# Optimization experiments

Measured on AMD Instinct MI355X. Metric: run time of the kernel, lower is better.

Reference implementation:

```python
import jax, jax.numpy as jnp
import numpy as np

N_SIDE = 14          # ViT-S/16 on 224x224 -> 14x14 patches
D_BACKBONE = 384
D_MODEL = 512
B_CLIPS = 32
T_FRAMES = 64
BT = B_CLIPS * T_FRAMES
LN_EPS = 1e-5


def setup_inputs() -> dict:
    key = jax.random.key(0)
    k0, k1, k2, k3, k4 = jax.random.split(key, 5)
    patch_tokens = jax.random.normal(k0, (BT, N_SIDE * N_SIDE, D_BACKBONE), dtype=jnp.float32)
    raw = jax.random.uniform(k1, (BT, 4), dtype=jnp.float32)
    # make well-formed boxes: x1<=x2, y1<=y2 (module clamps anyway)
    xy1 = jnp.minimum(raw[:, :2], raw[:, 2:])
    xy2 = jnp.maximum(raw[:, :2], raw[:, 2:])
    bboxes = jnp.concatenate([xy1, xy2], axis=1)
    obj_visible = jax.random.bernoulli(k2, 0.9, (BT,)).astype(jnp.float32)
    W = jax.random.normal(k3, (D_BACKBONE, D_MODEL), dtype=jnp.float32) * 0.02
    b = jnp.zeros((D_MODEL,), dtype=jnp.float32)
    gamma = jnp.ones((D_MODEL,), dtype=jnp.float32)
    beta = jnp.zeros((D_MODEL,), dtype=jnp.float32)
    mask_token = jax.random.normal(k4, (1, D_MODEL), dtype=jnp.float32) * 0.02
    return {"patch_tokens": patch_tokens, "bboxes": bboxes, "obj_visible": obj_visible,
            "B": B_CLIPS, "T": T_FRAMES, "W": W, "b": b, "gamma": gamma, "beta": beta,
            "mask_token": mask_token}


def _roi_mean_pool(patch_tokens, bboxes):
    bt, N, D = patch_tokens.shape
    n = N_SIDE
    grid = patch_tokens.reshape(bt, n, n, D)
    # exact replica of torch index math (clamp -> trunc/ceil -> clamp -> max)
    x1 = jnp.clip(bboxes[:, 0] * n, 0, n - 1).astype(jnp.int32)
    y1 = jnp.clip(bboxes[:, 1] * n, 0, n - 1).astype(jnp.int32)
    x2 = jnp.clip(jnp.ceil(jnp.clip(bboxes[:, 2] * n, 0, n)), 1, n).astype(jnp.int32)
    y2 = jnp.clip(jnp.ceil(jnp.clip(bboxes[:, 3] * n, 0, n)), 1, n).astype(jnp.int32)
    x2 = jnp.maximum(x2, x1 + 1)
    y2 = jnp.maximum(y2, y1 + 1)
    idx = jnp.arange(n)
    my = (idx[None, :] >= y1[:, None]) & (idx[None, :] < y2[:, None])  # [BT, n]
    mx = (idx[None, :] >= x1[:, None]) & (idx[None, :] < x2[:, None])  # [BT, n]
    mask = (my[:, :, None] & mx[:, None, :]).astype(grid.dtype)        # [BT, n, n]
    count = ((y2 - y1) * (x2 - x1)).astype(grid.dtype)                 # >= 1 always
    pooled = jnp.einsum('bhw,bhwd->bd', mask, grid) / count[:, None]
    return pooled


def reference(patch_tokens, bboxes, obj_visible, B, T, W, b, gamma, beta, mask_token):
    pooled = _roi_mean_pool(patch_tokens, bboxes)          # [BT, D_backbone]
    out = pooled @ W + b                                   # [BT, d_model]
    mu = jnp.mean(out, axis=-1, keepdims=True)
    var = jnp.mean(jnp.square(out - mu), axis=-1, keepdims=True)
    out = (out - mu) * jax.lax.rsqrt(var + LN_EPS) * gamma + beta
    vis = obj_visible[:, None]
    out = vis * out + (1.0 - vis) * mask_token             # learnable mask token blend
    return out.reshape(B, T, -1)
```

## Files before the change

### kernel.cpp

```cpp
#include <hip/hip_runtime.h>
#include <hip/hip_bf16.h>

#define N_SIDE 14
#define N_PATCH (N_SIDE * N_SIDE)
#define D_BB 384
#define DQ_BB (D_BB / 4)
#define D_MODEL 512
#define BT_TOTAL 2048
#define LN_EPS 1e-5f
#define PGROUPS 8
#define KSTEPS (D_BB / 32)

typedef __attribute__((ext_vector_type(8))) short bf16x8;
typedef __attribute__((ext_vector_type(4))) float f32x4;

__device__ __forceinline__ unsigned short f2b(float f) {
    unsigned u = __float_as_uint(f);
    return (unsigned short)((u + 0x7FFFu + ((u >> 16) & 1u)) >> 16);
}

__device__ __forceinline__ void add4(float4& a, const float4& b) {
    a.x += b.x; a.y += b.y; a.z += b.z; a.w += b.w;
}

__device__ __forceinline__ void box_params(const float* __restrict__ bboxes, int bt,
                                           int& x1, int& y1, int& wd, int& total) {
    const float bx1 = bboxes[bt * 4 + 0];
    const float by1 = bboxes[bt * 4 + 1];
    const float bx2 = bboxes[bt * 4 + 2];
    const float by2 = bboxes[bt * 4 + 3];
    x1 = (int)fminf(fmaxf(bx1 * (float)N_SIDE, 0.f), (float)(N_SIDE - 1));
    y1 = (int)fminf(fmaxf(by1 * (float)N_SIDE, 0.f), (float)(N_SIDE - 1));
    int x2 = (int)fminf(fmaxf(ceilf(fminf(fmaxf(bx2 * (float)N_SIDE, 0.f), (float)N_SIDE)), 1.f), (float)N_SIDE);
    int y2 = (int)fminf(fmaxf(ceilf(fminf(fmaxf(by2 * (float)N_SIDE, 0.f), (float)N_SIDE)), 1.f), (float)N_SIDE);
    x2 = max(x2, x1 + 1);
    y2 = max(y2, y1 + 1);
    wd = x2 - x1;
    total = wd * (y2 - y1);
}

__global__ __launch_bounds__(768) void pool_kernel(
    const float* __restrict__ patch,
    const float* __restrict__ bboxes,
    const float* __restrict__ W,
    unsigned short* __restrict__ pooled_bf,
    unsigned short* __restrict__ wpack)
{
    const int bt = blockIdx.x;
    const int t  = threadIdx.x;
    const int qd = t % DQ_BB;
    const int g  = t / DQ_BB;

    __shared__ int    off_tab[N_PATCH];
    __shared__ float4 part[PGROUPS][DQ_BB];

    if (bt < 64) {
        const int nt   = bt >> 1;
        const int kh   = bt & 1;
        const int lane = t & 63;
        const int grp  = t >> 6;
        const int ksl  = grp >> 1;
        const int jh   = grp & 1;
        const int ks   = kh * 6 + ksl;
        const int n    = nt * 16 + (lane & 15);
        const int kb   = ks * 32 + (lane >> 4) * 8 + jh * 4;
        ushort4 w4;
        w4.x = f2b(W[(size_t)(kb + 0) * D_MODEL + n]);
        w4.y = f2b(W[(size_t)(kb + 1) * D_MODEL + n]);
        w4.z = f2b(W[(size_t)(kb + 2) * D_MODEL + n]);
        w4.w = f2b(W[(size_t)(kb + 3) * D_MODEL + n]);
        *(ushort4*)(wpack + ((size_t)(nt * KSTEPS + ks) * 64 + lane) * 8 + jh * 4) = w4;
    }

    int x1, y1, wd, total;
    box_params(bboxes, bt, x1, y1, wd, total);
    const float inv_count = 1.f / (float)total;
    const float inv_wd = 1.f / (float)wd;
    const int cell0 = y1 * N_SIDE + x1;

    if (t < total) {
        const int y = (int)(((float)t + 0.5f) * inv_wd);
        const int x = t - y * wd;
        off_tab[t] = (cell0 + y * N_SIDE + x) * (DQ_BB * 16);
    }
    __syncthreads();

    const char* __restrict__ basep =
        (const char*)patch + (size_t)bt * N_PATCH * D_BB * 4 + (size_t)qd * 16;

    float4 acc = make_float4(0.f, 0.f, 0.f, 0.f);
    int c = g;
    for (; c + 3 * PGROUPS < total; c += 4 * PGROUPS) {
        const int o0 = off_tab[c];
        const int o1 = off_tab[c + PGROUPS];
        const int o2 = off_tab[c + 2 * PGROUPS];
        const int o3 = off_tab[c + 3 * PGROUPS];
        const float4 v0 = *(const float4*)(basep + o0);
        const float4 v1 = *(const float4*)(basep + o1);
        const float4 v2 = *(const float4*)(basep + o2);
        const float4 v3 = *(const float4*)(basep + o3);
        acc.x += (v0.x + v1.x) + (v2.x + v3.x);
        acc.y += (v0.y + v1.y) + (v2.y + v3.y);
        acc.z += (v0.z + v1.z) + (v2.z + v3.z);
        acc.w += (v0.w + v1.w) + (v2.w + v3.w);
    }
    for (; c < total; c += PGROUPS) {
        const float4 v = *(const float4*)(basep + off_tab[c]);
        acc.x += v.x; acc.y += v.y; acc.z += v.z; acc.w += v.w;
    }

    part[g][qd] = acc;
    __syncthreads();

    if (t < DQ_BB) {
        float4 s = part[0][t];
#pragma unroll
        for (int p = 1; p < PGROUPS; ++p) add4(s, part[p][t]);
        ushort4 o;
        o.x = f2b(s.x * inv_count);
        o.y = f2b(s.y * inv_count);
        o.z = f2b(s.z * inv_count);
        o.w = f2b(s.w * inv_count);
        *(ushort4*)(pooled_bf + (size_t)bt * D_BB + t * 4) = o;
    }
}

__global__ __launch_bounds__(512) void mfma_ln_kernel(
    const unsigned short* __restrict__ pooled_bf,
    const unsigned short* __restrict__ wpack,
    const float* __restrict__ bias,
    const float* __restrict__ gamma,
    const float* __restrict__ beta,
    const float* __restrict__ mask_tok,
    const float* __restrict__ vis,
    float* __restrict__ out)
{
    const int tid    = threadIdx.x;
    const int ch     = tid >> 6;
    const int lane   = tid & 63;
    const int lane_m = lane & 15;
    const int lane_g = lane >> 4;
    const int mrow0  = blockIdx.x * 16;

    bf16x8 afrag[KSTEPS];
    {
        const unsigned short* Arow = pooled_bf + (size_t)(mrow0 + lane_m) * D_BB + lane_g * 8;
#pragma unroll
        for (int ks = 0; ks < KSTEPS; ++ks)
            afrag[ks] = *(const bf16x8*)(Arow + ks * 32);
    }

    f32x4 acc[4];
#pragma unroll
    for (int nt = 0; nt < 4; ++nt) acc[nt] = (f32x4){0.f, 0.f, 0.f, 0.f};

#pragma unroll
    for (int nt = 0; nt < 4; ++nt) {
        const unsigned short* bp = wpack + ((size_t)((ch * 4 + nt) * KSTEPS) * 64 + lane) * 8;
#pragma unroll
        for (int ks = 0; ks < KSTEPS; ++ks) {
            const bf16x8 b = *(const bf16x8*)(bp + (size_t)ks * 64 * 8);
            acc[nt] = __builtin_amdgcn_mfma_f32_16x16x32_bf16(afrag[ks], b, acc[nt], 0, 0, 0);
        }
    }

    float s[4] = {0.f, 0.f, 0.f, 0.f}, s2[4] = {0.f, 0.f, 0.f, 0.f};
#pragma unroll
    for (int nt = 0; nt < 4; ++nt) {
        const float bs = bias[ch * 64 + nt * 16 + lane_m];
#pragma unroll
        for (int r = 0; r < 4; ++r) {
            const float v = acc[nt][r] + bs;
            acc[nt][r] = v;
            s[r] += v; s2[r] += v * v;
        }
    }
#pragma unroll
    for (int off = 1; off < 16; off <<= 1) {
#pragma unroll
        for (int r = 0; r < 4; ++r) {
            s[r]  += __shfl_xor(s[r],  off);
            s2[r] += __shfl_xor(s2[r], off);
        }
    }

    __shared__ float lns[8][16][2];
    if (lane_m == 0) {
#pragma unroll
        for (int r = 0; r < 4; ++r) {
            lns[ch][lane_g * 4 + r][0] = s[r];
            lns[ch][lane_g * 4 + r][1] = s2[r];
        }
    }
    __syncthreads();

    float mean4[4], rstd4[4], v4[4], iv4[4];
#pragma unroll
    for (int r = 0; r < 4; ++r) {
        const int m = lane_g * 4 + r;
        float S = 0.f, S2 = 0.f;
#pragma unroll
        for (int c = 0; c < 8; ++c) { S += lns[c][m][0]; S2 += lns[c][m][1]; }
        const float mean = S * (1.f / (float)D_MODEL);
        const float var  = S2 * (1.f / (float)D_MODEL) - mean * mean;
        mean4[r] = mean;
        rstd4[r] = rsqrtf(var + LN_EPS);
        const float v = vis[mrow0 + m];
        v4[r] = v; iv4[r] = 1.f - v;
    }

#pragma unroll
    for (int nt = 0; nt < 4; ++nt) {
        const int n = ch * 64 + nt * 16 + lane_m;
        const float gm  = gamma[n];
        const float bt_ = beta[n];
        const float mt  = mask_tok[n];
#pragma unroll
        for (int r = 0; r < 4; ++r) {
            const int row = mrow0 + lane_g * 4 + r;
            const float o = v4[r] * ((acc[nt][r] - mean4[r]) * rstd4[r] * gm + bt_) + iv4[r] * mt;
            out[(size_t)row * D_MODEL + n] = o;
        }
    }
}

extern "C" void kernel_launch(void* const* d_in, const int* in_sizes, int n_in,
                              void* d_out, int out_size, void* d_ws, size_t ws_size,
                              hipStream_t stream) {
    const float* patch  = (const float*)d_in[0];
    const float* bboxes = (const float*)d_in[1];
    const float* vis    = (const float*)d_in[2];
    const float* W      = (const float*)d_in[5];
    const float* bias   = (const float*)d_in[6];
    const float* gamma  = (const float*)d_in[7];
    const float* beta   = (const float*)d_in[8];
    const float* mtok   = (const float*)d_in[9];

    unsigned short* pooled_bf = (unsigned short*)d_ws;
    unsigned short* wpack     = (unsigned short*)((char*)d_ws + (2u << 20));
    float* out = (float*)d_out;

    pool_kernel<<<BT_TOTAL, 768, 0, stream>>>(patch, bboxes, W, pooled_bf, wpack);
    mfma_ln_kernel<<<BT_TOTAL / 16, 512, 0, stream>>>(
        pooled_bf, wpack, bias, gamma, beta, mtok, vis, out);
}
```

Before: 32.12 us.

## Fuse ROI pooling into MFMA+LayerNorm kernel with 4 rows per block

Moves the W bf16 packing into a small separate kernel. ROI mean pooling now runs inside the GEMM/LayerNorm kernel: each block pools 4 rows sequentially into shared memory, zero-pads them to a 16-row MFMA tile, and writes only the 4 valid rows. This removes the pooled intermediate round-trip through global memory. In exchange, the gather runs with fewer threads per row, behind serial barriers, and 12 of the 16 MFMA rows do wasted work.

```diff
diff --git a/kernel.cpp b/kernel.cpp
--- a/kernel.cpp
+++ b/kernel.cpp
@@ -8,8 +8,9 @@
 #define D_MODEL 512
 #define BT_TOTAL 2048
 #define LN_EPS 1e-5f
-#define PGROUPS 8
 #define KSTEPS (D_BB / 32)
+#define PGR 5
+#define ALDS_P 392
 
 typedef __attribute__((ext_vector_type(8))) short bf16x8;
 typedef __attribute__((ext_vector_type(4))) float f32x4;
@@ -39,31 +40,24 @@
     total = wd * (y2 - y1);
 }
 
-__global__ __launch_bounds__(768) void pool_kernel(
-    const float* __restrict__ patch,
-    const float* __restrict__ bboxes,
+__global__ __launch_bounds__(192) void wpack_kernel(
     const float* __restrict__ W,
-    unsigned short* __restrict__ pooled_bf,
     unsigned short* __restrict__ wpack)
 {
-    const int bt = blockIdx.x;
-    const int t  = threadIdx.x;
-    const int qd = t % DQ_BB;
-    const int g  = t / DQ_BB;
-
-    __shared__ int    off_tab[N_PATCH];
-    __shared__ float4 part[PGROUPS][DQ_BB];
-
-    if (bt < 64) {
-        const int nt   = bt >> 1;
-        const int kh   = bt & 1;
-        const int lane = t & 63;
-        const int grp  = t >> 6;
-        const int ksl  = grp >> 1;
-        const int jh   = grp & 1;
-        const int ks   = kh * 6 + ksl;
-        const int n    = nt * 16 + (lane & 15);
-        const int kb   = ks * 32 + (lane >> 4) * 8 + jh * 4;
+    const int bid  = blockIdx.x;
+    const int t    = threadIdx.x;
+    const int nt   = bid >> 1;
+    const int kh   = bid & 1;
+    const int lane = t & 63;
+    const int w3   = t >> 6;
+#pragma unroll
+    for (int u = 0; u < 4; ++u) {
+        const int grp = w3 * 4 + u;
+        const int ksl = grp >> 1;
+        const int jh  = grp & 1;
+        const int ks  = kh * 6 + ksl;
+        const int n   = nt * 16 + (lane & 15);
+        const int kb  = ks * 32 + (lane >> 4) * 8 + jh * 4;
         ushort4 w4;
         w4.x = f2b(W[(size_t)(kb + 0) * D_MODEL + n]);
         w4.y = f2b(W[(size_t)(kb + 1) * D_MODEL + n]);
@@ -71,62 +65,11 @@
         w4.w = f2b(W[(size_t)(kb + 3) * D_MODEL + n]);
         *(ushort4*)(wpack + ((size_t)(nt * KSTEPS + ks) * 64 + lane) * 8 + jh * 4) = w4;
     }
-
-    int x1, y1, wd, total;
-    box_params(bboxes, bt, x1, y1, wd, total);
-    const float inv_count = 1.f / (float)total;
-    const float inv_wd = 1.f / (float)wd;
-    const int cell0 = y1 * N_SIDE + x1;
-
-    if (t < total) {
-        const int y = (int)(((float)t + 0.5f) * inv_wd);
-        const int x = t - y * wd;
-        off_tab[t] = (cell0 + y * N_SIDE + x) * (DQ_BB * 16);
-    }
-    __syncthreads();
-
-    const char* __restrict__ basep =
-        (const char*)patch + (size_t)bt * N_PATCH * D_BB * 4 + (size_t)qd * 16;
-
-    float4 acc = make_float4(0.f, 0.f, 0.f, 0.f);
-    int c = g;
-    for (; c + 3 * PGROUPS < total; c += 4 * PGROUPS) {
-        const int o0 = off_tab[c];
-        const int o1 = off_tab[c + PGROUPS];
-        const int o2 = off_tab[c + 2 * PGROUPS];
-        const int o3 = off_tab[c + 3 * PGROUPS];
-        const float4 v0 = *(const float4*)(basep + o0);
-        const float4 v1 = *(const float4*)(basep + o1);
-        const float4 v2 = *(const float4*)(basep + o2);
-        const float4 v3 = *(const float4*)(basep + o3);
-        acc.x += (v0.x + v1.x) + (v2.x + v3.x);
-        acc.y += (v0.y + v1.y) + (v2.y + v3.y);
-        acc.z += (v0.z + v1.z) + (v2.z + v3.z);
-        acc.w += (v0.w + v1.w) + (v2.w + v3.w);
-    }
-    for (; c < total; c += PGROUPS) {
-        const float4 v = *(const float4*)(basep + off_tab[c]);
-        acc.x += v.x; acc.y += v.y; acc.z += v.z; acc.w += v.w;
-    }
-
-    part[g][qd] = acc;
-    __syncthreads();
-
-    if (t < DQ_BB) {
-        float4 s = part[0][t];
-#pragma unroll
-        for (int p = 1; p < PGROUPS; ++p) add4(s, part[p][t]);
-        ushort4 o;
-        o.x = f2b(s.x * inv_count);
-        o.y = f2b(s.y * inv_count);
-        o.z = f2b(s.z * inv_count);
-        o.w = f2b(s.w * inv_count);
-        *(ushort4*)(pooled_bf + (size_t)bt * D_BB + t * 4) = o;
-    }
-}
-
-__global__ __launch_bounds__(512) void mfma_ln_kernel(
-    const unsigned short* __restrict__ pooled_bf,
+}
+
+__global__ __launch_bounds__(512) void fused_kernel(
+    const float* __restrict__ patch,
+    const float* __restrict__ bboxes,
     const unsigned short* __restrict__ wpack,
     const float* __restrict__ bias,
     const float* __restrict__ gamma,
@@ -135,20 +78,87 @@
     const float* __restrict__ vis,
     float* __restrict__ out)
 {
-    const int tid    = threadIdx.x;
+    const int tid = threadIdx.x;
+    const int r0  = blockIdx.x * 4;
+    const int qd  = tid % DQ_BB;
+    const int g   = tid / DQ_BB;
+
+    __shared__ int            off_tab[N_PATCH];
+    __shared__ float4         part[PGR][DQ_BB];
+    __shared__ unsigned short alds[16][ALDS_P];
+    __shared__ float          lns[8][16][2];
+
+    {
+        ushort4 z; z.x = z.y = z.z = z.w = 0;
+        ushort4* a4 = (ushort4*)alds;
+        for (int i = tid; i < 16 * (ALDS_P / 4); i += 512) a4[i] = z;
+    }
+
+    for (int r = 0; r < 4; ++r) {
+        int x1, y1, wd, total;
+        box_params(bboxes, r0 + r, x1, y1, wd, total);
+        const float inv_wd    = 1.f / (float)wd;
+        const float inv_count = 1.f / (float)total;
+        const int   cell0     = y1 * N_SIDE + x1;
+
+        __syncthreads();
+        if (tid < total) {
+            const int y = (int)(((float)tid + 0.5f) * inv_wd);
+            const int x = tid - y * wd;
+            off_tab[tid] = (cell0 + y * N_SIDE + x) * (D_BB * 4);
+        }
+        __syncthreads();
+
+        if (tid < PGR * DQ_BB) {
+            const char* __restrict__ basep =
+                (const char*)patch + (size_t)(r0 + r) * N_PATCH * D_BB * 4 + (size_t)qd * 16;
+            float4 acc = make_float4(0.f, 0.f, 0.f, 0.f);
+            int c = g;
+            for (; c + 3 * PGR < total; c += 4 * PGR) {
+                const int o0 = off_tab[c];
+                const int o1 = off_tab[c + PGR];
+                const int o2 = off_tab[c + 2 * PGR];
+                const int o3 = off_tab[c + 3 * PGR];
+                const float4 v0 = *(const float4*)(basep + o0);
+                const float4 v1 = *(const float4*)(basep + o1);
+                const float4 v2 = *(const float4*)(basep + o2);
+                const float4 v3 = *(const float4*)(basep + o3);
+                acc.x += (v0.x + v1.x) + (v2.x + v3.x);
+                acc.y += (v0.y + v1.y) + (v2.y + v3.y);
+                acc.z += (v0.z + v1.z) + (v2.z + v3.z);
+                acc.w += (v0.w + v1.w) + (v2.w + v3.w);
+            }
+            for (; c < total; c += PGR) {
+                const float4 v = *(const float4*)(basep + off_tab[c]);
+                acc.x += v.x; acc.y += v.y; acc.z += v.z; acc.w += v.w;
+            }
+            part[g][qd] = acc;
+        }
+        __syncthreads();
+
+        if (tid < DQ_BB) {
+            float4 s = part[0][tid];
+#pragma unroll
+            for (int p = 1; p < PGR; ++p) add4(s, part[p][tid]);
+            ushort4 o;
+            o.x = f2b(s.x * inv_count);
+            o.y = f2b(s.y * inv_count);
+            o.z = f2b(s.z * inv_count);
+            o.w = f2b(s.w * inv_count);
+            *(ushort4*)&alds[r][tid * 4] = o;
+        }
+    }
+    __syncthreads();
+
     const int ch     = tid >> 6;
     const int lane   = tid & 63;
     const int lane_m = lane & 15;
     const int lane_g = lane >> 4;
-    const int mrow0  = blockIdx.x * 16;
 
     bf16x8 afrag[KSTEPS];
-    {
-        const unsigned short* Arow = pooled_bf + (size_t)(mrow0 + lane_m) * D_BB + lane_g * 8;
-#pragma unroll
-        for (int ks = 0; ks < KSTEPS; ++ks)
-            afrag[ks] = *(const bf16x8*)(Arow + ks * 32);
-    }
+#pragma unroll
+    for (int ks = 0; ks < KSTEPS; ++ks)
+        afrag[ks] = *(const bf16x8*)&alds[lane_m][ks * 32 + lane_g * 8];
 
     f32x4 acc[4];
 #pragma unroll
@@ -183,8 +193,6 @@
             s2[r] += __shfl_xor(s2[r], off);
         }
     }
-
-    __shared__ float lns[8][16][2];
     if (lane_m == 0) {
 #pragma unroll
         for (int r = 0; r < 4; ++r) {
@@ -194,32 +202,31 @@
     }
     __syncthreads();
 
-    float mean4[4], rstd4[4], v4[4], iv4[4];
-#pragma unroll
-    for (int r = 0; r < 4; ++r) {
-        const int m = lane_g * 4 + r;
-        float S = 0.f, S2 = 0.f;
-#pragma unroll
-        for (int c = 0; c < 8; ++c) { S += lns[c][m][0]; S2 += lns[c][m][1]; }
-        const float mean = S * (1.f / (float)D_MODEL);
-        const float var  = S2 * (1.f / (float)D_MODEL) - mean * mean;
-        mean4[r] = mean;
-        rstd4[r] = rsqrtf(var + LN_EPS);
-        const float v = vis[mrow0 + m];
-        v4[r] = v; iv4[r] = 1.f - v;
-    }
-
-#pragma unroll
-    for (int nt = 0; nt < 4; ++nt) {
-        const int n = ch * 64 + nt * 16 + lane_m;
-        const float gm  = gamma[n];
-        const float bt_ = beta[n];
-        const float mt  = mask_tok[n];
-#pragma unroll
-        for (int r = 0; r < 4; ++r) {
-            const int row = mrow0 + lane_g * 4 + r;
-            const float o = v4[r] * ((acc[nt][r] - mean4[r]) * rstd4[r] * gm + bt_) + iv4[r] * mt;
-            out[(size_t)row * D_MODEL + n] = o;
+    if (lane_g == 0) {
+        float mean4[4], rstd4[4], v4[4], iv4[4];
+#pragma unroll
+        for (int r = 0; r < 4; ++r) {
+            float S = 0.f, S2 = 0.f;
+#pragma unroll
+            for (int c = 0; c < 8; ++c) { S += lns[c][r][0]; S2 += lns[c][r][1]; }
+            const float mean = S * (1.f / (float)D_MODEL);
+            const float var  = S2 * (1.f / (float)D_MODEL) - mean * mean;
+            mean4[r] = mean;
+            rstd4[r] = rsqrtf(var + LN_EPS);
+            const float v = vis[r0 + r];
+            v4[r] = v; iv4[r] = 1.f - v;
+        }
+#pragma unroll
+        for (int nt = 0; nt < 4; ++nt) {
+            const int n = ch * 64 + nt * 16 + lane_m;
+            const float gm  = gamma[n];
+            const float bt_ = beta[n];
+            const float mt  = mask_tok[n];
+#pragma unroll
+            for (int r = 0; r < 4; ++r) {
+                const float o = v4[r] * ((acc[nt][r] - mean4[r]) * rstd4[r] * gm + bt_) + iv4[r] * mt;
+                out[(size_t)(r0 + r) * D_MODEL + n] = o;
+            }
         }
     }
 }
@@ -236,11 +243,10 @@
     const float* beta   = (const float*)d_in[8];
     const float* mtok   = (const float*)d_in[9];
 
-    unsigned short* pooled_bf = (unsigned short*)d_ws;
-    unsigned short* wpack     = (unsigned short*)((char*)d_ws + (2u << 20));
+    unsigned short* wpack = (unsigned short*)d_ws;
     float* out = (float*)d_out;
 
-    pool_kernel<<<BT_TOTAL, 768, 0, stream>>>(patch, bboxes, W, pooled_bf, wpack);
-    mfma_ln_kernel<<<BT_TOTAL / 16, 512, 0, stream>>>(
-        pooled_bf, wpack, bias, gamma, beta, mtok, vis, out);
-}
+    wpack_kernel<<<64, 192, 0, stream>>>(W, wpack);
+    fused_kernel<<<BT_TOTAL / 4, 512, 0, stream>>>(
+        patch, bboxes, wpack, bias, gamma, beta, mtok, vis, out);
+}
```

Result: slower. 36.58 us (+13.9%).
